# Kernel tuning notes

Hardware: AMD Instinct MI355X
Metric: run time of the kernel (lower is better)

## Reference

```python
import jax, jax.numpy as jnp
import numpy as np

N_EMBD = 512
Q_N_EMBD = 512
N_HEAD = 8
EPS = 1e-5


def _layernorm(x, w, b):
    mu = jnp.mean(x, axis=-1, keepdims=True)
    var = jnp.mean(jnp.square(x - mu), axis=-1, keepdims=True)
    return (x - mu) * jax.lax.rsqrt(var + EPS) * w + b


def setup_inputs() -> dict:
    key = jax.random.key(0)
    ks = jax.random.split(key, 16)
    B, C, H, W = 8, N_EMBD, 32, 32
    s = 1.0 / np.sqrt(N_EMBD)
    inp = {
        "q": jax.random.normal(ks[0], (B, Q_N_EMBD, H, W), jnp.float32),
        "kv": jax.random.normal(ks[1], (B, C, H, W), jnp.float32),
        "ln_kv_w": jnp.ones((N_EMBD,), jnp.float32),
        "ln_kv_b": jnp.zeros((N_EMBD,), jnp.float32),
        "ln_q_w": jnp.ones((Q_N_EMBD,), jnp.float32),
        "ln_q_b": jnp.zeros((Q_N_EMBD,), jnp.float32),
        "Wk": jax.random.normal(ks[2], (N_EMBD, N_EMBD), jnp.float32) * s,
        "bk": jnp.zeros((N_EMBD,), jnp.float32),
        "Wq": jax.random.normal(ks[3], (Q_N_EMBD, N_EMBD), jnp.float32) * s,
        "bq": jnp.zeros((N_EMBD,), jnp.float32),
        "Wv": jax.random.normal(ks[4], (N_EMBD, N_EMBD), jnp.float32) * s,
        "bv": jnp.zeros((N_EMBD,), jnp.float32),
        "Wp": jax.random.normal(ks[5], (N_EMBD, N_EMBD), jnp.float32) * s,
        "bp": jnp.zeros((N_EMBD,), jnp.float32),
    }
    return inp


def reference(q, kv, ln_kv_w, ln_kv_b, ln_q_w, ln_q_b,
              Wk, bk, Wq, bq, Wv, bv, Wp, bp):
    B, C, H, W = kv.shape
    c_q = q.shape[1]
    T = H * W
    hd = C // N_HEAD  # head dim

    # [B, C, H, W] -> [B, T, C] tokens
    kv_t = kv.reshape(B, C, T).transpose(0, 2, 1)
    q_t = q.reshape(B, c_q, T).transpose(0, 2, 1)

    kv_n = _layernorm(kv_t, ln_kv_w, ln_kv_b)
    q_n = _layernorm(q_t, ln_q_w, ln_q_b)

    # projections, split heads: [B, T, C] -> [B, H, T, hd]
    def heads(x):
        return x.reshape(B, T, N_HEAD, hd).transpose(0, 2, 1, 3)

    k = heads(kv_n @ Wk + bk)
    qh = heads(q_n @ Wq + bq)
    v = heads(kv_n @ Wv + bv)

    att = jnp.einsum('bhqd,bhkd->bhqk', qh, k) * (1.0 / np.sqrt(hd))
    att = jax.nn.softmax(att, axis=-1)
    y = jnp.einsum('bhqk,bhkd->bhqd', att, v)
    y = y.transpose(0, 2, 1, 3).reshape(B, T, C)
    y = y @ Wp + bp

    x = kv_t + y  # residual on (pre-LN) kv tokens
    return x.transpose(0, 2, 1).reshape(B, C, H, W)
```

## Files before the change

### kernel.cpp

```cpp
#include <hip/hip_runtime.h>
#include <stdint.h>

#define DI static __device__ __forceinline__

typedef __attribute__((ext_vector_type(8))) short bh8;
typedef __attribute__((ext_vector_type(4))) float f4;

DI short f2bf(float f) {
  unsigned u = __float_as_uint(f);
  u += 0x7fffu + ((u >> 16) & 1u);
  return (short)(u >> 16);
}

DI unsigned pkbf(float a, float b) {
  unsigned ua = __float_as_uint(a) + 0x8000u;
  unsigned ub = __float_as_uint(b) + 0x8000u;
  return __builtin_amdgcn_perm(ub, ua, 0x07060302u);
}

DI unsigned pk4fp8(float a, float b, float c, float d) {
  unsigned w = 0;
  w = __builtin_amdgcn_cvt_pk_fp8_f32(a, b, w, false);
  w = __builtin_amdgcn_cvt_pk_fp8_f32(c, d, w, true);
  return w;
}

DI void gll16(const void* g, void* l) {
  __builtin_amdgcn_global_load_lds(
      (const __attribute__((address_space(1))) unsigned int*)g,
      (__attribute__((address_space(3))) unsigned int*)l, 16, 0, 0);
}

DI void fence_vm_lgkm() {
  asm volatile("s_waitcnt vmcnt(0) lgkmcnt(0)" ::: "memory");
}

DI f4 mfma16(bh8 a, bh8 b, f4 c) {
  return __builtin_amdgcn_mfma_f32_16x16x32_bf16(a, b, c, 0, 0, 0);
}

DI f4 mfma8(long a, long b, f4 c) {
  return __builtin_amdgcn_mfma_f32_16x16x32_fp8_fp8(a, b, c, 0, 0, 0);
}

DI bh8 ld8(const short* p) { return *(const bh8*)p; }

__global__ __launch_bounds__(256) void prep_k(
    const float* __restrict__ kv, const float* __restrict__ qi,
    const float* __restrict__ kw, const float* __restrict__ kbv,
    const float* __restrict__ qw, const float* __restrict__ qbv,
    const float* __restrict__ Wk, const float* __restrict__ Wq,
    const float* __restrict__ Wv, const float* __restrict__ Wp,
    short* __restrict__ kvn, short* __restrict__ qn,
    short* __restrict__ Wt)
{
  __shared__ char sm[16 * 516 * 4 + 128];
  int role = blockIdx.y;
  int bx = blockIdx.x;
  int tid = threadIdx.x;

  if (role < 4) {
    if (bx >= 256) return;
    float (*ts)[33] = (float(*)[33])sm;
    const float* w = (role == 0) ? Wk : (role == 1) ? Wq : (role == 2) ? Wv : Wp;
    short* o = Wt + ((size_t)role << 18);
    int c0 = (bx & 15) << 5, r0 = (bx >> 4) << 5;
    int tx = tid & 31, ty = tid >> 5;
#pragma unroll
    for (int k = 0; k < 32; k += 8)
      ts[ty + k][tx] = w[((size_t)(r0 + ty + k) << 9) + c0 + tx];
    __syncthreads();
#pragma unroll
    for (int k = 0; k < 32; k += 8)
      o[((size_t)(c0 + ty + k) << 9) + r0 + tx] = f2bf(ts[tx][ty + k]);
    return;
  }

  float (*xs)[516] = (float(*)[516])sm;
  float* smean = (float*)(sm + 16 * 516 * 4);
  float* srstd = smean + 16;
  int which = role - 4;
  const float* x = which ? qi : kv;
  const float* w = which ? qw : kw;
  const float* bb = which ? qbv : kbv;
  short* o = which ? qn : kvn;
  int b = bx >> 6;
  int t0 = (bx & 63) << 4;
  const float* xb = x + ((size_t)b << 19) + (size_t)t0;
#pragma unroll
  for (int k = 0; k < 8; k++) {
    int idx = (k << 8) + tid;
    int c = idx >> 2, tt = (idx & 3) << 2;
    float4 v = *(const float4*)(xb + ((size_t)c << 10) + tt);
    xs[tt + 0][c] = v.x; xs[tt + 1][c] = v.y;
    xs[tt + 2][c] = v.z; xs[tt + 3][c] = v.w;
  }
  __syncthreads();
  {
    int t = tid >> 4, cp = tid & 15;
    float s = 0.f, s2 = 0.f;
#pragma unroll
    for (int k = 0; k < 8; k++) {
      float4 v = *(const float4*)&xs[t][(cp << 2) + (k << 6)];
      s  += v.x + v.y + v.z + v.w;
      s2 += v.x * v.x + v.y * v.y + v.z * v.z + v.w * v.w;
    }
#pragma unroll
    for (int m = 1; m < 16; m <<= 1) {
      s  += __shfl_xor(s,  m);
      s2 += __shfl_xor(s2, m);
    }
    if (cp == 0) {
      float mean = s * (1.f / 512.f);
      float var  = s2 * (1.f / 512.f) - mean * mean;
      smean[t] = mean;
      srstd[t] = rsqrtf(var + 1e-5f);
    }
  }
  __syncthreads();
#pragma unroll
  for (int k = 0; k < 8; k++) {
    int idx = (k << 8) + tid;
    int t = idx >> 7, c = (idx & 127) << 2;
    float4 v = *(const float4*)&xs[t][c];
    float4 wv = *(const float4*)(w + c);
    float4 bv4 = *(const float4*)(bb + c);
    float mu = smean[t], rs = srstd[t];
    float r0 = (v.x - mu) * rs * wv.x + bv4.x;
    float r1 = (v.y - mu) * rs * wv.y + bv4.y;
    float r2 = (v.z - mu) * rs * wv.z + bv4.z;
    float r3 = (v.w - mu) * rs * wv.w + bv4.w;
    uint2 pk; pk.x = pkbf(r0, r1); pk.y = pkbf(r2, r3);
    *(uint2*)(o + (((size_t)(b << 10) + t0 + t) << 9) + c) = pk;
  }
}

__global__ __launch_bounds__(256, 2) void gemm_qkv_k(
    const short* __restrict__ kvn, const short* __restrict__ qn,
    const short* __restrict__ Wt,
    const float* __restrict__ bk, const float* __restrict__ bq,
    const float* __restrict__ bv,
    unsigned char* __restrict__ kb8, unsigned char* __restrict__ qb8,
    unsigned char* __restrict__ vb8)
{
  __shared__ short As[2][128 * 64];
  __shared__ short Bs[2][128 * 64];
  int z = blockIdx.z;
  const short* A; const short* Bt; const float* bias;
  int m0, n0;
  if (z == 0)      { A = Wt;             Bt = kvn;            bias = bk; }
  else if (z == 1) { A = Wt + (1 << 18); Bt = qn;             bias = bq; }
  else             { A = kvn;            Bt = Wt + (2 << 18); bias = bv; }
  if (z == 2) { m0 = blockIdx.x << 7; n0 = blockIdx.y << 7; }
  else        { m0 = blockIdx.y << 7; n0 = blockIdx.x << 7; }
  int tid = threadIdx.x;
  int lane = tid & 63, wid = tid >> 6;
  int r = lane & 15, g = lane >> 4;
  int wrow = (wid >> 1) << 6, wcol = (wid & 1) << 6;

  auto STAGE = [&](int k0, int s) {
#pragma unroll
    for (int it = 0; it < 4; it++) {
      int n = (it << 8) + tid;
      int row = n >> 3;
      int c = (n & 7) ^ (row & 7);
      gll16(A  + ((size_t)(m0 + row) << 9) + k0 + (c << 3), &As[s][n << 3]);
      gll16(Bt + ((size_t)(n0 + row) << 9) + k0 + (c << 3), &Bs[s][n << 3]);
    }
  };

  f4 acc[4][4];
#pragma unroll
  for (int i = 0; i < 4; i++)
#pragma unroll
    for (int j = 0; j < 4; j++) {
      acc[i][j][0] = 0.f; acc[i][j][1] = 0.f;
      acc[i][j][2] = 0.f; acc[i][j][3] = 0.f;
    }

  STAGE(0, 0);
  fence_vm_lgkm();
  __builtin_amdgcn_s_barrier();
  __builtin_amdgcn_sched_barrier(0);

  for (int kt = 0; kt < 8; kt++) {
    int cur = kt & 1;
    if (kt < 7) STAGE((kt + 1) << 6, cur ^ 1);
    const short* Ap = As[cur];
    const short* Bp = Bs[cur];
    bh8 a[2][4], b[2][4];
#pragma unroll
    for (int ks = 0; ks < 2; ks++) {
#pragma unroll
      for (int i = 0; i < 4; i++) {
        int R = wrow + (i << 4) + r;
        a[ks][i] = ld8(Ap + (R << 6) + ((((ks << 2) + g) ^ (R & 7)) << 3));
      }
#pragma unroll
      for (int j = 0; j < 4; j++) {
        int R = wcol + (j << 4) + r;
        b[ks][j] = ld8(Bp + (R << 6) + ((((ks << 2) + g) ^ (R & 7)) << 3));
      }
    }
#pragma unroll
    for (int ks = 0; ks < 2; ks++)
#pragma unroll
      for (int i = 0; i < 4; i++)
#pragma unroll
        for (int j = 0; j < 4; j++)
          acc[i][j] = mfma16(a[ks][i], b[ks][j], acc[i][j]);
    if (kt < 7) {
      fence_vm_lgkm();
      __builtin_amdgcn_s_barrier();
      __builtin_amdgcn_sched_barrier(0);
    }
  }
#pragma unroll
  for (int i = 0; i < 4; i++) {
#pragma unroll
    for (int j = 0; j < 4; j++) {
      int mm = m0 + wrow + (i << 4) + (g << 2);
      int nn = n0 + wcol + (j << 4) + r;
      if (z == 0) {
        float4 b4 = *(const float4*)(bias + mm);
        int h = mm >> 6, d0 = mm & 63;
        int bb = nn >> 10, tt = nn & 1023;
        int c = tt & 255;
        int p = ((c & 15) << 4) | (c >> 4);
        size_t base = ((size_t)((bb * 8 + h) * 4 + (tt >> 8)) << 14);
        unsigned w = pk4fp8(acc[i][j][0] + b4.x, acc[i][j][1] + b4.y,
                            acc[i][j][2] + b4.z, acc[i][j][3] + b4.w);
        *(unsigned*)(kb8 + base + (p << 6) +
                     (((d0 >> 3) ^ (p & 7)) << 3) + (d0 & 7)) = w;
      } else if (z == 1) {
        float4 b4 = *(const float4*)(bias + mm);
        int h = mm >> 6, d0 = mm & 63;
        int bb = nn >> 10, tt = nn & 1023;
        unsigned w = pk4fp8(acc[i][j][0] + b4.x, acc[i][j][1] + b4.y,
                            acc[i][j][2] + b4.z, acc[i][j][3] + b4.w);
        *(unsigned*)(qb8 + ((((size_t)(bb * 8 + h)) << 10) + tt) * 64 + d0) = w;
      } else {
        float bvv = bias[nn];
        int h = nn >> 6, d = nn & 63;
        int bb = mm >> 10, tt = mm & 1023;
        int t8 = tt & 255;
        int tb = (((t8 >> 4) & 3) << 3) | (((t8 >> 3) & 1) << 2) | (t8 >> 6);
        size_t base = ((size_t)((bb * 8 + h) * 4 + (tt >> 8)) << 14);
        unsigned w = pk4fp8(acc[i][j][0] + bvv, acc[i][j][1] + bvv,
                            acc[i][j][2] + bvv, acc[i][j][3] + bvv);
        *(unsigned*)(vb8 + base + (d << 8) +
                     ((tb ^ (d & 31)) << 3) + (tt & 7)) = w;
      }
    }
  }
}

__global__ __launch_bounds__(256, 3) void gemm_proj_k(
    const short* __restrict__ A, const short* __restrict__ Bt,
    const float* __restrict__ bias, float* __restrict__ outp,
    const float* __restrict__ resid)
{
  __shared__ short As[2][64 * 64];
  __shared__ short Bs[2][128 * 64];
  int m0 = blockIdx.y << 6, n0 = blockIdx.x << 7;
  int tid = threadIdx.x;
  int lane = tid & 63, wid = tid >> 6;
  int r = lane & 15, g = lane >> 4;
  int wrow = (wid >> 1) << 5, wcol = (wid & 1) << 6;

  auto STAGE = [&](int k0, int s) {
#pragma unroll
    for (int it = 0; it < 2; it++) {
      int n = (it << 8) + tid;
      int row = n >> 3;
      int c = (n & 7) ^ (row & 7);
      gll16(A + ((size_t)(m0 + row) << 9) + k0 + (c << 3), &As[s][n << 3]);
    }
#pragma unroll
    for (int it = 0; it < 4; it++) {
      int n = (it << 8) + tid;
      int row = n >> 3;
      int c = (n & 7) ^ (row & 7);
      gll16(Bt + ((size_t)(n0 + row) << 9) + k0 + (c << 3), &Bs[s][n << 3]);
    }
  };

  f4 acc[2][4];
#pragma unroll
  for (int i = 0; i < 2; i++)
#pragma unroll
    for (int j = 0; j < 4; j++) {
      acc[i][j][0] = 0.f; acc[i][j][1] = 0.f;
      acc[i][j][2] = 0.f; acc[i][j][3] = 0.f;
    }

  STAGE(0, 0);
  fence_vm_lgkm();
  __builtin_amdgcn_s_barrier();
  __builtin_amdgcn_sched_barrier(0);

  for (int kt = 0; kt < 8; kt++) {
    int cur = kt & 1;
    if (kt < 7) STAGE((kt + 1) << 6, cur ^ 1);
    const short* Ap = As[cur];
    const short* Bp = Bs[cur];
    bh8 a[2][2], b[2][4];
#pragma unroll
    for (int ks = 0; ks < 2; ks++) {
#pragma unroll
      for (int i = 0; i < 2; i++) {
        int R = wrow + (i << 4) + r;
        a[ks][i] = ld8(Ap + (R << 6) + ((((ks << 2) + g) ^ (R & 7)) << 3));
      }
#pragma unroll
      for (int j = 0; j < 4; j++) {
        int R = wcol + (j << 4) + r;
        b[ks][j] = ld8(Bp + (R << 6) + ((((ks << 2) + g) ^ (R & 7)) << 3));
      }
    }
#pragma unroll
    for (int ks = 0; ks < 2; ks++)
#pragma unroll
      for (int i = 0; i < 2; i++)
#pragma unroll
        for (int j = 0; j < 4; j++)
          acc[i][j] = mfma16(a[ks][i], b[ks][j], acc[i][j]);
    if (kt < 7) {
      fence_vm_lgkm();
      __builtin_amdgcn_s_barrier();
      __builtin_amdgcn_sched_barrier(0);
    }
  }
#pragma unroll
  for (int i = 0; i < 2; i++) {
#pragma unroll
    for (int j = 0; j < 4; j++) {
      int mm = m0 + wrow + (i << 4) + (g << 2);
      int nn = n0 + wcol + (j << 4) + r;
      int bb = nn >> 10, t = nn & 1023;
#pragma unroll
      for (int q = 0; q < 4; q++) {
        int m = mm + q;
        size_t ad = ((((size_t)bb << 9) + m) << 10) + t;
        outp[ad] = acc[i][j][q] + bias[m] + resid[ad];
      }
    }
  }
}

__global__ __launch_bounds__(256, 2) void attn_k(
    const unsigned char* __restrict__ qb8, const unsigned char* __restrict__ kb8,
    const unsigned char* __restrict__ vb8, short* __restrict__ yo)
{
  __shared__ char Ks[2][16384];
  __shared__ char Vs[2][16384];
  int h = blockIdx.x, b = blockIdx.z;
  int qt0 = blockIdx.y << 6;
  int tid = threadIdx.x, lane = tid & 63;
  int r = lane & 15, g = lane >> 4;
  int wbase = (tid >> 6) << 4;
  size_t bh = (size_t)(b * 8 + h);
  const unsigned char* Qg = qb8 + ((bh << 10) + qt0) * 64;
  const unsigned char* Kg = kb8 + (bh << 16);
  const unsigned char* Vg = vb8 + (bh << 16);

  auto STAGE = [&](int ck, int s) {
#pragma unroll
    for (int it = 0; it < 4; it++) {
      int n = ((it << 8) + tid) << 4;
      gll16(Kg + (ck << 14) + n, &Ks[s][n]);
      gll16(Vg + (ck << 14) + n, &Vs[s][n]);
    }
  };

  long qf8[2];
#pragma unroll
  for (int ksd = 0; ksd < 2; ksd++)
    qf8[ksd] = *(const long*)(Qg +
        ((size_t)(wbase + r) << 6) + (((ksd << 2) + g) << 3));

  f4 oac[4];
#pragma unroll
  for (int jn = 0; jn < 4; jn++) {
    oac[jn][0] = 0.f; oac[jn][1] = 0.f; oac[jn][2] = 0.f; oac[jn][3] = 0.f;
  }
  float rs = 0.f;

  const float csc = 0.18033688011112042f;

  STAGE(0, 0);
  fence_vm_lgkm();
  __builtin_amdgcn_s_barrier();
  __builtin_amdgcn_sched_barrier(0);

  for (int ck = 0; ck < 4; ck++) {
    int cur = ck & 1;
    if (ck < 3) STAGE(ck + 1, cur ^ 1);
    const char* Kp = Ks[cur];
    const char* Vp = Vs[cur];

    unsigned Wq[4][4];
#pragma unroll
    for (int jq = 0; jq < 4; jq++) {
      f4 s[4];
#pragma unroll
      for (int jj = 0; jj < 4; jj++) {
        s[jj][0] = 0.f; s[jj][1] = 0.f; s[jj][2] = 0.f; s[jj][3] = 0.f;
      }
#pragma unroll
      for (int ksd = 0; ksd < 2; ksd++)
#pragma unroll
        for (int jj = 0; jj < 4; jj++) {
          int j = (jq << 2) + jj;
          long kf = *(const long*)(Kp + (((j << 4) + r) << 6) +
                        ((((ksd << 2) + g) ^ (r & 7)) << 3));
          s[jj] = mfma8(kf, qf8[ksd], s[jj]);
        }
#pragma unroll
      for (int qq = 0; qq < 4; qq++) {
        float e0 = __builtin_amdgcn_exp2f(fminf(fmaf(s[0][qq], csc, -3.0f), 8.5f));
        float e1 = __builtin_amdgcn_exp2f(fminf(fmaf(s[1][qq], csc, -3.0f), 8.5f));
        float e2 = __builtin_amdgcn_exp2f(fminf(fmaf(s[2][qq], csc, -3.0f), 8.5f));
        float e3 = __builtin_amdgcn_exp2f(fminf(fmaf(s[3][qq], csc, -3.0f), 8.5f));
        rs += (e0 + e1) + (e2 + e3);
        Wq[qq][jq] = pk4fp8(e0, e1, e2, e3);
      }
    }

#pragma unroll
    for (int ks = 0; ks < 8; ks++) {
      long ap = (long)(unsigned)Wq[ks >> 1][(ks & 1) << 1] |
                ((long)Wq[ks >> 1][((ks & 1) << 1) + 1] << 32);
#pragma unroll
      for (int jn = 0; jn < 4; jn++) {
        int d = (jn << 4) + r;
        long bv8 = *(const long*)(Vp + (d << 8) +
                      ((((ks << 2) + g) ^ (d & 31)) << 3));
        oac[jn] = mfma8(ap, bv8, oac[jn]);
      }
    }

    if (ck < 3) {
      fence_vm_lgkm();
      __builtin_amdgcn_s_barrier();
      __builtin_amdgcn_sched_barrier(0);
    }
  }

  rs += __shfl_xor(rs, 16);
  rs += __shfl_xor(rs, 32);

#pragma unroll
  for (int qq = 0; qq < 4; qq++) {
    float rsq = __shfl(rs, (g << 2) + qq);
    float inv = 1.f / (rsq + 1e-20f);
    int trow = qt0 + wbase + (g << 2) + qq;
    size_t base = (((size_t)(b << 10) + trow) << 9) + (h << 6);
#pragma unroll
    for (int jn = 0; jn < 4; jn++)
      yo[base + (jn << 4) + r] = f2bf(oac[jn][qq] * inv);
  }
}

extern "C" void kernel_launch(void* const* d_in, const int* in_sizes, int n_in,
                              void* d_out, int out_size, void* d_ws, size_t ws_size,
                              hipStream_t stream)
{
  const float* q    = (const float*)d_in[0];
  const float* kv   = (const float*)d_in[1];
  const float* lnkw = (const float*)d_in[2];
  const float* lnkb = (const float*)d_in[3];
  const float* lnqw = (const float*)d_in[4];
  const float* lnqb = (const float*)d_in[5];
  const float* Wk   = (const float*)d_in[6];
  const float* bk   = (const float*)d_in[7];
  const float* Wq   = (const float*)d_in[8];
  const float* bq   = (const float*)d_in[9];
  const float* Wv   = (const float*)d_in[10];
  const float* bv   = (const float*)d_in[11];
  const float* Wp   = (const float*)d_in[12];
  const float* bp   = (const float*)d_in[13];

  char* ws = (char*)d_ws;
  const size_t SZ = (size_t)8192 * 512 * 2;
  short* buf0 = (short*)(ws);
  short* qn   = (short*)(ws + SZ);
  unsigned char* kb8 = (unsigned char*)(ws + 2 * SZ);
  unsigned char* qb8 = (unsigned char*)(ws + 3 * SZ);
  unsigned char* vb8 = (unsigned char*)(ws + 4 * SZ);
  short* Wt   = (short*)(ws + 5 * SZ);
  if (ws_size < 5 * SZ + 4 * 512 * 512 * 2) return;

  prep_k<<<dim3(512, 6), 256, 0, stream>>>(kv, q, lnkw, lnkb, lnqw, lnqb,
                                           Wk, Wq, Wv, Wp, buf0, qn, Wt);
  gemm_qkv_k<<<dim3(64, 4, 3), 256, 0, stream>>>(buf0, qn, Wt, bk, bq, bv,
                                                 kb8, qb8, vb8);
  attn_k<<<dim3(8, 16, 8), 256, 0, stream>>>(qb8, kb8, vb8, buf0);
  gemm_proj_k<<<dim3(64, 8), 256, 0, stream>>>(Wt + (3 << 18), buf0, bp,
                                               (float*)d_out, kv);
}
```

Baseline: 176.2 us.

## Use partial vmcnt waits so next-stage prefetch overlaps compute in GEMM and attention loops

```diff
diff --git a/kernel.cpp b/kernel.cpp
--- a/kernel.cpp
+++ b/kernel.cpp
@@ -31,9 +31,9 @@
       (__attribute__((address_space(3))) unsigned int*)l, 16, 0, 0);
 }
 
-DI void fence_vm_lgkm() {
-  asm volatile("s_waitcnt vmcnt(0) lgkmcnt(0)" ::: "memory");
-}
+DI void waitvm8() { asm volatile("s_waitcnt vmcnt(8)" ::: "memory"); }
+DI void waitvm6() { asm volatile("s_waitcnt vmcnt(6)" ::: "memory"); }
+DI void waitvm0() { asm volatile("s_waitcnt vmcnt(0)" ::: "memory"); }
 
 DI f4 mfma16(bh8 a, bh8 b, f4 c) {
   return __builtin_amdgcn_mfma_f32_16x16x32_bf16(a, b, c, 0, 0, 0);
@@ -179,13 +179,14 @@
     }
 
   STAGE(0, 0);
-  fence_vm_lgkm();
-  __builtin_amdgcn_s_barrier();
-  __builtin_amdgcn_sched_barrier(0);
-
+#pragma unroll
   for (int kt = 0; kt < 8; kt++) {
     int cur = kt & 1;
     if (kt < 7) STAGE((kt + 1) << 6, cur ^ 1);
+    __builtin_amdgcn_sched_barrier(0);
+    if (kt < 7) waitvm8(); else waitvm0();
+    __builtin_amdgcn_s_barrier();
+    __builtin_amdgcn_sched_barrier(0);
     const short* Ap = As[cur];
     const short* Bp = Bs[cur];
     bh8 a[2][4], b[2][4];
@@ -209,11 +210,8 @@
 #pragma unroll
         for (int j = 0; j < 4; j++)
           acc[i][j] = mfma16(a[ks][i], b[ks][j], acc[i][j]);
-    if (kt < 7) {
-      fence_vm_lgkm();
-      __builtin_amdgcn_s_barrier();
-      __builtin_amdgcn_sched_barrier(0);
-    }
+    __builtin_amdgcn_sched_barrier(0);
+    if (kt < 7) __builtin_amdgcn_s_barrier();
   }
 #pragma unroll
   for (int i = 0; i < 4; i++) {
@@ -295,13 +293,14 @@
     }
 
   STAGE(0, 0);
-  fence_vm_lgkm();
-  __builtin_amdgcn_s_barrier();
-  __builtin_amdgcn_sched_barrier(0);
-
+#pragma unroll
   for (int kt = 0; kt < 8; kt++) {
     int cur = kt & 1;
     if (kt < 7) STAGE((kt + 1) << 6, cur ^ 1);
+    __builtin_amdgcn_sched_barrier(0);
+    if (kt < 7) waitvm6(); else waitvm0();
+    __builtin_amdgcn_s_barrier();
+    __builtin_amdgcn_sched_barrier(0);
     const short* Ap = As[cur];
     const short* Bp = Bs[cur];
     bh8 a[2][2], b[2][4];
@@ -325,11 +324,8 @@
 #pragma unroll
         for (int j = 0; j < 4; j++)
           acc[i][j] = mfma16(a[ks][i], b[ks][j], acc[i][j]);
-    if (kt < 7) {
-      fence_vm_lgkm();
-      __builtin_amdgcn_s_barrier();
-      __builtin_amdgcn_sched_barrier(0);
-    }
+    __builtin_amdgcn_sched_barrier(0);
+    if (kt < 7) __builtin_amdgcn_s_barrier();
   }
 #pragma unroll
   for (int i = 0; i < 2; i++) {
@@ -389,13 +385,14 @@
   const float csc = 0.18033688011112042f;
 
   STAGE(0, 0);
-  fence_vm_lgkm();
-  __builtin_amdgcn_s_barrier();
-  __builtin_amdgcn_sched_barrier(0);
-
+#pragma unroll
   for (int ck = 0; ck < 4; ck++) {
     int cur = ck & 1;
     if (ck < 3) STAGE(ck + 1, cur ^ 1);
+    __builtin_amdgcn_sched_barrier(0);
+    if (ck < 3) waitvm8(); else waitvm0();
+    __builtin_amdgcn_s_barrier();
+    __builtin_amdgcn_sched_barrier(0);
     const char* Kp = Ks[cur];
     const char* Vp = Vs[cur];
 
@@ -440,11 +437,8 @@
       }
     }
 
-    if (ck < 3) {
-      fence_vm_lgkm();
-      __builtin_amdgcn_s_barrier();
-      __builtin_amdgcn_sched_barrier(0);
-    }
+    __builtin_amdgcn_sched_barrier(0);
+    if (ck < 3) __builtin_amdgcn_s_barrier();
   }
 
   rs += __shfl_xor(rs, 16);
```

Measured after the change: 197.7 us. 12.2% more time.
